# Kernel optimization log

Measured on AMD Instinct MI355X. Metric: run time of the kernel, lower is better.

## Reference

```python
import jax, jax.numpy as jnp
import numpy as np

N = 50000          # num_nodes
E = 1600000        # num directed edges
IN_C = 128         # in_channels
OUT_C = 128        # out_channels
HEADS = 8
HFD = OUT_C // HEADS  # head_feat_dim = 16
NEG_SLOPE = 0.2


def setup_inputs() -> dict:
    key = jax.random.key(0)
    k1, k2, k3, k4, k5 = jax.random.split(key, 5)
    node_feats = jax.random.normal(k1, (N, IN_C), dtype=jnp.float32)
    edge_index = jax.random.randint(k2, (2, E), 0, N, dtype=jnp.int64)
    # parameters (xavier-ish scale, kept small so exp() stays in range)
    W = jax.random.normal(k3, (OUT_C, IN_C), dtype=jnp.float32) * (1.0 / np.sqrt(IN_C))
    a_left = jax.random.normal(k4, (HFD, HEADS), dtype=jnp.float32) * 0.1
    a_right = jax.random.normal(k5, (HFD, HEADS), dtype=jnp.float32) * 0.1
    bias = jnp.zeros((OUT_C,), dtype=jnp.float32)
    return {"node_feats": node_feats, "edge_index": edge_index,
            "W": W, "a_left": a_left, "a_right": a_right, "bias": bias}


def reference(node_feats, edge_index, W, a_left, a_right, bias):
    n = node_feats.shape[0]
    # embedding: Linear without bias, then split into heads -> [n, h, c]
    emb = (node_feats @ W.T).reshape(n, HEADS, HFD)
    # per-node attention logit halves: sum_c emb[n,h,c] * a[c,h] -> [n, h]
    left = jnp.einsum('nhc,ch->nh', emb, a_left)
    right = jnp.einsum('nhc,ch->nh', emb, a_right)
    src = edge_index[0]
    dst = edge_index[1]
    # edge logit: score(src, dst) uses a_left on src, a_right on dst
    e = left[src] + right[dst]                       # [E, h]
    e = jnp.where(e >= 0, e, NEG_SLOPE * e)          # leaky relu(0.2)
    w = jnp.exp(e)                                   # [E, h] (module uses raw exp)
    denom = jax.ops.segment_sum(w, dst, num_segments=n)  # [n, h]
    attn = w / denom[dst]                            # [E, h]
    msg = emb[src] * attn[:, :, None]                # [E, h, c]
    out = jax.ops.segment_sum(msg, dst, num_segments=n)  # [n, h, c]
    # concat heads + bias
    out = out.reshape(n, HEADS * HFD) + bias
    return out
```

## Files before the change

kernel.cpp:

```cpp
#include <hip/hip_runtime.h>
#include <hip/hip_bf16.h>

#define N_NODES 50000
#define N_EDGES 1600000
#define HEADS 8
#define HFD 16
#define CH 128

#define PART 128
#define NB 391
#define BCAP 5120
#define PA_T 512
#define PA_CHUNK 3200
#define PA_PER 7
#define PA_BLOCKS 500
#define EMB_BLOCKS 391

#define QPART 32
#define QCAP 1536
#define AG_TASKS (NB * 4)
#define AG_BLOCKS 1568

typedef __bf16 bf16x8 __attribute__((ext_vector_type(8)));
typedef __bf16 bf16x4 __attribute__((ext_vector_type(4)));
typedef float f32x4 __attribute__((ext_vector_type(4)));
typedef float f32x2 __attribute__((ext_vector_type(2)));

__device__ __forceinline__ float bf_lo(unsigned u) { return __uint_as_float(u << 16); }
__device__ __forceinline__ float bf_hi(unsigned u) { return __uint_as_float(u & 0xffff0000u); }

__global__ __launch_bounds__(256) void k_splitw(const float* __restrict__ W,
                                                const float* __restrict__ aL,
                                                const float* __restrict__ aR,
                                                __bf16* __restrict__ Whi,
                                                __bf16* __restrict__ Wlo,
                                                __bf16* __restrict__ Vhi,
                                                __bf16* __restrict__ Vlo,
                                                int* __restrict__ bucket_cnt) {
  int t = blockIdx.x * 256 + threadIdx.x;
  if (t < NB) bucket_cnt[t] = 0;
  if (t < CH * CH / 4) {
    f32x4 v = ((const f32x4*)W)[t];
    bf16x4 h, l;
#pragma unroll
    for (int i = 0; i < 4; ++i) {
      __bf16 hb = (__bf16)v[i];
      h[i] = hb;
      l[i] = (__bf16)(v[i] - (float)hb);
    }
    ((bf16x4*)Whi)[t] = h;
    ((bf16x4*)Wlo)[t] = l;
  }
  if (t < 16 * CH) {
    int j = t >> 7;
    int k = t & 127;
    int h = j & 7;
    const float* a = (j < 8) ? aL : aR;
    float v = 0.f;
#pragma unroll
    for (int c = 0; c < HFD; ++c) v += W[(h * HFD + c) * CH + k] * a[c * HEADS + h];
    __bf16 hb = (__bf16)v;
    Vhi[t] = hb;
    Vlo[t] = (__bf16)(v - (float)hb);
  }
}

__global__ __launch_bounds__(PA_T) void k_prep(const int* __restrict__ ei,
                                               int* __restrict__ bucket_cnt,
                                               unsigned* __restrict__ ebuf,
                                               const float* __restrict__ X,
                                               const __bf16* __restrict__ Whi,
                                               const __bf16* __restrict__ Wlo,
                                               const __bf16* __restrict__ Vhi,
                                               const __bf16* __restrict__ Vlo,
                                               __bf16* __restrict__ embb,
                                               float* __restrict__ leftp,
                                               float* __restrict__ rightp) {
  __shared__ unsigned sp[PA_CHUNK];
  __shared__ int hist[NB];
  __shared__ int lcur[NB];
  __shared__ int wbase[NB];
  __shared__ int wpart[8];
  int t = threadIdx.x;

  if (blockIdx.x >= PA_BLOCKS) {
    int ntile = (blockIdx.x - PA_BLOCKS) * 8 + (t >> 6);
    if (ntile >= N_NODES / 16) return;
    int lane = t & 63;
    int c = lane & 15, quad = lane >> 4;
    const float* xp = X + (size_t)(ntile * 16 + c) * CH + quad * 8;
    bf16x8 xh[4], xl[4];
#pragma unroll
    for (int ks = 0; ks < 4; ++ks) {
      float4 x0 = *(const float4*)(xp + ks * 32);
      float4 x1 = *(const float4*)(xp + ks * 32 + 4);
      float xv[8] = {x0.x, x0.y, x0.z, x0.w, x1.x, x1.y, x1.z, x1.w};
#pragma unroll
      for (int j = 0; j < 8; ++j) {
        __bf16 hb = (__bf16)xv[j];
        xh[ks][j] = hb;
        xl[ks][j] = (__bf16)(xv[j] - (float)hb);
      }
    }
#pragma unroll
    for (int h = 0; h < HEADS; ++h) {
      const __bf16* wp = Whi + (size_t)(h * 16 + c) * CH + quad * 8;
      const __bf16* wlp = Wlo + (size_t)(h * 16 + c) * CH + quad * 8;
      f32x4 acc = {0.f, 0.f, 0.f, 0.f};
#pragma unroll
      for (int ks = 0; ks < 4; ++ks) {
        bf16x8 wh = *(const bf16x8*)(wp + ks * 32);
        bf16x8 wl = *(const bf16x8*)(wlp + ks * 32);
        acc = __builtin_amdgcn_mfma_f32_16x16x32_bf16(xl[ks], wh, acc, 0, 0, 0);
        acc = __builtin_amdgcn_mfma_f32_16x16x32_bf16(xh[ks], wl, acc, 0, 0, 0);
        acc = __builtin_amdgcn_mfma_f32_16x16x32_bf16(xh[ks], wh, acc, 0, 0, 0);
      }
#pragma unroll
      for (int r = 0; r < 4; ++r) {
        int node = ntile * 16 + quad * 4 + r;
        embb[(size_t)node * CH + h * HFD + c] = (__bf16)acc[r];
      }
    }
    {
      const __bf16* vp = Vhi + (size_t)c * CH + quad * 8;
      const __bf16* vlp = Vlo + (size_t)c * CH + quad * 8;
      f32x4 acc = {0.f, 0.f, 0.f, 0.f};
#pragma unroll
      for (int ks = 0; ks < 4; ++ks) {
        bf16x8 vh = *(const bf16x8*)(vp + ks * 32);
        bf16x8 vl = *(const bf16x8*)(vlp + ks * 32);
        acc = __builtin_amdgcn_mfma_f32_16x16x32_bf16(xl[ks], vh, acc, 0, 0, 0);
        acc = __builtin_amdgcn_mfma_f32_16x16x32_bf16(xh[ks], vl, acc, 0, 0, 0);
        acc = __builtin_amdgcn_mfma_f32_16x16x32_bf16(xh[ks], vh, acc, 0, 0, 0);
      }
#pragma unroll
      for (int r = 0; r < 4; ++r) {
        int node = ntile * 16 + quad * 4 + r;
        if (c < 8) leftp[node * HEADS + c] = acc[r];
        else rightp[node * HEADS + (c - 8)] = acc[r];
      }
    }
    return;
  }

  int base = blockIdx.x * PA_CHUNK;
  for (int i = t; i < NB; i += PA_T) hist[i] = 0;
  __syncthreads();
  unsigned pk[PA_PER];
#pragma unroll
  for (int i = 0; i < PA_PER; ++i) {
    int e = t + i * PA_T;
    pk[i] = 0xffffffffu;
    if (e < PA_CHUNK) {
      int src = ei[base + e];
      int dst = ei[N_EDGES + base + e];
      pk[i] = ((unsigned)(dst >> 7) << 23) | ((unsigned)(dst & 127) << 16) |
              (unsigned)src;
      atomicAdd(&hist[dst >> 7], 1);
    }
  }
  __syncthreads();
  int hv = (t < NB) ? hist[t] : 0;
  int lane = t & 63, wid = t >> 6;
  int v = hv;
#pragma unroll
  for (int d = 1; d < 64; d <<= 1) {
    int o = __shfl_up(v, d);
    if (lane >= d) v += o;
  }
  if (lane == 63) wpart[wid] = v;
  __syncthreads();
  if (t < 8) {
    int pv = wpart[t];
#pragma unroll
    for (int d = 1; d < 8; d <<= 1) {
      int o = __shfl_up(pv, d);
      if (t >= d) pv += o;
    }
    wpart[t] = pv;
  }
  __syncthreads();
  int val = v + ((wid > 0) ? wpart[wid - 1] : 0);
  if (t < NB) {
    int lstart = val - hv;
    lcur[t] = lstart;
    int prior = hv ? atomicAdd(&bucket_cnt[t], hv) : 0;
    wbase[t] = t * BCAP + prior - lstart;
  }
  __syncthreads();
#pragma unroll
  for (int i = 0; i < PA_PER; ++i) {
    if (pk[i] != 0xffffffffu) {
      int b = pk[i] >> 23;
      int pos = atomicAdd(&lcur[b], 1);
      sp[pos] = pk[i];
    }
  }
  __syncthreads();
  for (int i = t; i < PA_CHUNK; i += PA_T) {
    unsigned p = sp[i];
    int b = p >> 23;
    int slot = wbase[b] + i;
    if (slot < (b + 1) * BCAP) ebuf[slot] = p;
  }
}

__global__ __launch_bounds__(256) void k_aggr(const int* __restrict__ bucket_cnt,
                                              const unsigned* __restrict__ ebuf,
                                              const __bf16* __restrict__ embb,
                                              const float* __restrict__ leftp,
                                              const float* __restrict__ rightp,
                                              const float* __restrict__ bias,
                                              float* __restrict__ out) {
  __shared__ unsigned short su[QCAP];
  __shared__ int hist[QPART];
  __shared__ int pfx[QPART];
  __shared__ int cur[QPART];
  int T = (blockIdx.x & 7) * (AG_BLOCKS / 8) + (blockIdx.x >> 3);
  if (T >= AG_TASKS) return;
  int b = T >> 2;
  int q = T & 3;
  int t = threadIdx.x;
  int cnt = bucket_cnt[b];
  if (cnt > BCAP) cnt = BCAP;
  int ebase = b * BCAP;
  if (t < QPART) hist[t] = 0;
  __syncthreads();
  for (int e4 = t * 4; e4 < cnt; e4 += 1024) {
    uint4 pp = *(const uint4*)(ebuf + ebase + e4);
    unsigned pj[4] = {pp.x, pp.y, pp.z, pp.w};
#pragma unroll
    for (int j = 0; j < 4; ++j) {
      if (e4 + j < cnt) {
        int dl = (pj[j] >> 16) & 127;
        if ((dl >> 5) == q) atomicAdd(&hist[dl & 31], 1);
      }
    }
  }
  __syncthreads();
  if (t < 64) {
    int v = (t < QPART) ? hist[t] : 0;
#pragma unroll
    for (int d = 1; d < QPART; d <<= 1) {
      int o = __shfl_up(v, d);
      if (t >= d) v += o;
    }
    if (t < QPART) {
      int ex = v - hist[t];
      pfx[t] = ex;
      cur[t] = ex;
    }
  }
  __syncthreads();
  for (int e4 = t * 4; e4 < cnt; e4 += 1024) {
    uint4 pp = *(const uint4*)(ebuf + ebase + e4);
    unsigned pj[4] = {pp.x, pp.y, pp.z, pp.w};
#pragma unroll
    for (int j = 0; j < 4; ++j) {
      if (e4 + j < cnt) {
        unsigned p = pj[j];
        int dl = (p >> 16) & 127;
        if ((dl >> 5) == q) {
          int pos = atomicAdd(&cur[dl & 31], 1);
          if (pos < QCAP) su[pos] = (unsigned short)(p & 0xffffu);
        }
      }
    }
  }
  __syncthreads();

  int wv = t >> 6;
  int lane = t & 63;
  int g = lane >> 4;
  int m = lane & 15;
  int h = m >> 1;
#pragma unroll 1
  for (int k = 0; k < 8; ++k) {
    int dl = wv * 8 + k;
    int dst = b * PART + q * QPART + dl;
    bool valid = dst < N_NODES;
    int beg = pfx[dl];
    int cd = hist[dl];
    if (beg + cd > QCAP) cd = QCAP - beg;
    float r = valid ? rightp[dst * HEADS + h] : 0.f;
    f32x2 acc2[4];
    acc2[0] = (f32x2){0.f, 0.f};
    acc2[1] = (f32x2){0.f, 0.f};
    acc2[2] = (f32x2){0.f, 0.f};
    acc2[3] = (f32x2){0.f, 0.f};
    float dsum = 0.f;
    if (cd > 0) {
      int sA0, sA1, sB0, sB1, sC0, sC1;
      uint4 uA0, uA1, uB0, uB1, uC0, uC1;
      float lA0, lA1, lB0, lB1, lC0, lC1;
#define STAGE(E0, s0, s1, u0, u1, l0, l1)                          \
      {                                                            \
        int i0 = (E0) + g, i1 = (E0) + 4 + g;                      \
        s0 = su[beg + ((i0 < cd) ? i0 : 0)];                       \
        s1 = su[beg + ((i1 < cd) ? i1 : 0)];                       \
        u0 = ((const uint4*)(embb + (size_t)s0 * CH))[m];          \
        u1 = ((const uint4*)(embb + (size_t)s1 * CH))[m];          \
        l0 = leftp[s0 * HEADS + h];                                \
        l1 = leftp[s1 * HEADS + h];                                \
      }
#define CONSUME(E0, u0, u1, l0, l1)                                \
      {                                                            \
        bool a0 = (E0) + g < cd, a1 = (E0) + 4 + g < cd;           \
        float x0 = l0 + r;                                         \
        x0 = (x0 >= 0.f) ? x0 : 0.2f * x0;                         \
        float w0 = a0 ? __expf(x0) : 0.f;                          \
        float x1 = l1 + r;                                         \
        x1 = (x1 >= 0.f) ? x1 : 0.2f * x1;                         \
        float w1 = a1 ? __expf(x1) : 0.f;                          \
        dsum += w0 + w1;                                           \
        f32x2 wv0 = {w0, w0}, wv1 = {w1, w1};                      \
        acc2[0] += wv0 * (f32x2){bf_lo(u0.x), bf_hi(u0.x)}         \
                 + wv1 * (f32x2){bf_lo(u1.x), bf_hi(u1.x)};        \
        acc2[1] += wv0 * (f32x2){bf_lo(u0.y), bf_hi(u0.y)}         \
                 + wv1 * (f32x2){bf_lo(u1.y), bf_hi(u1.y)};        \
        acc2[2] += wv0 * (f32x2){bf_lo(u0.z), bf_hi(u0.z)}         \
                 + wv1 * (f32x2){bf_lo(u1.z), bf_hi(u1.z)};        \
        acc2[3] += wv0 * (f32x2){bf_lo(u0.w), bf_hi(u0.w)}         \
                 + wv1 * (f32x2){bf_lo(u1.w), bf_hi(u1.w)};        \
      }
      STAGE(0, sA0, sA1, uA0, uA1, lA0, lA1);
      __builtin_amdgcn_sched_barrier(0);
      if (8 < cd) STAGE(8, sB0, sB1, uB0, uB1, lB0, lB1);
      __builtin_amdgcn_sched_barrier(0);
      int e0 = 0;
      while (true) {
        if (e0 + 16 < cd) STAGE(e0 + 16, sC0, sC1, uC0, uC1, lC0, lC1);
        __builtin_amdgcn_sched_barrier(0);
        CONSUME(e0, uA0, uA1, lA0, lA1);
        e0 += 8;
        if (e0 >= cd) break;
        if (e0 + 16 < cd) STAGE(e0 + 16, sA0, sA1, uA0, uA1, lA0, lA1);
        __builtin_amdgcn_sched_barrier(0);
        CONSUME(e0, uB0, uB1, lB0, lB1);
        e0 += 8;
        if (e0 >= cd) break;
        if (e0 + 16 < cd) STAGE(e0 + 16, sB0, sB1, uB0, uB1, lB0, lB1);
        __builtin_amdgcn_sched_barrier(0);
        CONSUME(e0, uC0, uC1, lC0, lC1);
        e0 += 8;
        if (e0 >= cd) break;
      }
#undef STAGE
#undef CONSUME
    }
    float a0 = acc2[0].x, a1 = acc2[0].y, a2 = acc2[1].x, a3 = acc2[1].y;
    float a4 = acc2[2].x, a5 = acc2[2].y, a6 = acc2[3].x, a7 = acc2[3].y;
#pragma unroll
    for (int mask = 16; mask <= 32; mask <<= 1) {
      dsum += __shfl_xor(dsum, mask);
      a0 += __shfl_xor(a0, mask);
      a1 += __shfl_xor(a1, mask);
      a2 += __shfl_xor(a2, mask);
      a3 += __shfl_xor(a3, mask);
      a4 += __shfl_xor(a4, mask);
      a5 += __shfl_xor(a5, mask);
      a6 += __shfl_xor(a6, mask);
      a7 += __shfl_xor(a7, mask);
    }
    if (g == 0 && valid) {
      float inv = (dsum > 0.f) ? 1.0f / dsum : 0.f;
      float4 b0 = ((const float4*)bias)[2 * m];
      float4 b1 = ((const float4*)bias)[2 * m + 1];
      float4 o0 = {a0 * inv + b0.x, a1 * inv + b0.y,
                   a2 * inv + b0.z, a3 * inv + b0.w};
      float4 o1 = {a4 * inv + b1.x, a5 * inv + b1.y,
                   a6 * inv + b1.z, a7 * inv + b1.w};
      ((float4*)(out + (size_t)dst * CH))[2 * m] = o0;
      ((float4*)(out + (size_t)dst * CH))[2 * m + 1] = o1;
    }
  }
}

extern "C" void kernel_launch(void* const* d_in, const int* in_sizes, int n_in,
                              void* d_out, int out_size, void* d_ws, size_t ws_size,
                              hipStream_t stream) {
  const float* X = (const float*)d_in[0];
  const int* ei = (const int*)d_in[1];
  const float* W = (const float*)d_in[2];
  const float* al = (const float*)d_in[3];
  const float* ar = (const float*)d_in[4];
  const float* bias = (const float*)d_in[5];
  float* out = (float*)d_out;

  unsigned* ebuf = (unsigned*)d_ws;
  __bf16* embb = (__bf16*)(ebuf + (size_t)NB * BCAP);
  __bf16* Whi = embb + (size_t)N_NODES * CH;
  __bf16* Wlo = Whi + CH * CH;
  __bf16* Vhi = Wlo + CH * CH;
  __bf16* Vlo = Vhi + 16 * CH;
  float* leftp = (float*)(Vlo + 16 * CH);
  float* rightp = leftp + (size_t)N_NODES * HEADS;
  int* bucket_cnt = (int*)(rightp + (size_t)N_NODES * HEADS);

  k_splitw<<<16, 256, 0, stream>>>(W, al, ar, Whi, Wlo, Vhi, Vlo, bucket_cnt);
  k_prep<<<PA_BLOCKS + EMB_BLOCKS, PA_T, 0, stream>>>(ei, bucket_cnt, ebuf, X,
                                                      Whi, Wlo, Vhi, Vlo, embb,
                                                      leftp, rightp);
  k_aggr<<<AG_BLOCKS, 256, 0, stream>>>(bucket_cnt, ebuf, embb, leftp, rightp, bias, out);
}
```

Measured before the change: 206.4 us.

## Bin aggregation edges by source-node phase to improve gather locality across waves

The aggregation kernel now sorts each quarter-bucket's edges by destination and also by a coarse source-index phase (src>>14, four phases). Every wave keeps accumulators for all 8 of its destinations in registers and walks the phases in order. The aim is for concurrently running waves to gather embedding rows from the same region of memory, which should improve L2/cache hit rates. In exchange, the manual triple-buffered software prefetch pipeline is dropped in favour of a simple per-edge loop. The kernel also now holds 8x4 accumulators per lane and adds launch bounds of 4 blocks, which raises register pressure and the risk of spilling.

```diff
diff --git a/kernel.cpp b/kernel.cpp
--- a/kernel.cpp
+++ b/kernel.cpp
@@ -20,6 +20,10 @@
 #define QCAP 1536
 #define AG_TASKS (NB * 4)
 #define AG_BLOCKS 1568
+
+#define NPH 4
+#define PHSH 14
+#define NBIN (NPH * QPART)
 
 typedef __bf16 bf16x8 __attribute__((ext_vector_type(8)));
 typedef __bf16 bf16x4 __attribute__((ext_vector_type(4)));
@@ -205,17 +209,18 @@
   }
 }
 
-__global__ __launch_bounds__(256) void k_aggr(const int* __restrict__ bucket_cnt,
-                                              const unsigned* __restrict__ ebuf,
-                                              const __bf16* __restrict__ embb,
-                                              const float* __restrict__ leftp,
-                                              const float* __restrict__ rightp,
-                                              const float* __restrict__ bias,
-                                              float* __restrict__ out) {
+__global__ __launch_bounds__(256, 4) void k_aggr(const int* __restrict__ bucket_cnt,
+                                                 const unsigned* __restrict__ ebuf,
+                                                 const __bf16* __restrict__ embb,
+                                                 const float* __restrict__ leftp,
+                                                 const float* __restrict__ rightp,
+                                                 const float* __restrict__ bias,
+                                                 float* __restrict__ out) {
   __shared__ unsigned short su[QCAP];
-  __shared__ int hist[QPART];
-  __shared__ int pfx[QPART];
-  __shared__ int cur[QPART];
+  __shared__ int hist[NBIN];
+  __shared__ int pfx[NBIN];
+  __shared__ int cur[NBIN];
+  __shared__ int wp2[2];
   int T = (blockIdx.x & 7) * (AG_BLOCKS / 8) + (blockIdx.x >> 3);
   if (T >= AG_TASKS) return;
   int b = T >> 2;
@@ -224,7 +229,7 @@
   int cnt = bucket_cnt[b];
   if (cnt > BCAP) cnt = BCAP;
   int ebase = b * BCAP;
-  if (t < QPART) hist[t] = 0;
+  for (int i = t; i < NBIN; i += 256) hist[i] = 0;
   __syncthreads();
   for (int e4 = t * 4; e4 < cnt; e4 += 1024) {
     uint4 pp = *(const uint4*)(ebuf + ebase + e4);
@@ -233,23 +238,31 @@
     for (int j = 0; j < 4; ++j) {
       if (e4 + j < cnt) {
         int dl = (pj[j] >> 16) & 127;
-        if ((dl >> 5) == q) atomicAdd(&hist[dl & 31], 1);
-      }
-    }
-  }
-  __syncthreads();
-  if (t < 64) {
-    int v = (t < QPART) ? hist[t] : 0;
-#pragma unroll
-    for (int d = 1; d < QPART; d <<= 1) {
+        if ((dl >> 5) == q) {
+          int ph = (int)(pj[j] & 0xffffu) >> PHSH;
+          atomicAdd(&hist[ph * QPART + (dl & 31)], 1);
+        }
+      }
+    }
+  }
+  __syncthreads();
+  int hv = 0, vin = 0;
+  if (t < NBIN) {
+    hv = hist[t];
+    int v = hv;
+#pragma unroll
+    for (int d = 1; d < 64; d <<= 1) {
       int o = __shfl_up(v, d);
-      if (t >= d) v += o;
-    }
-    if (t < QPART) {
-      int ex = v - hist[t];
-      pfx[t] = ex;
-      cur[t] = ex;
-    }
+      if ((t & 63) >= d) v += o;
+    }
+    if ((t & 63) == 63) wp2[t >> 6] = v;
+    vin = v;
+  }
+  __syncthreads();
+  if (t < NBIN) {
+    int inc = vin + ((t >= 64) ? wp2[0] : 0);
+    pfx[t] = inc - hv;
+    cur[t] = inc - hv;
   }
   __syncthreads();
   for (int e4 = t * 4; e4 < cnt; e4 += 1024) {
@@ -261,7 +274,8 @@
         unsigned p = pj[j];
         int dl = (p >> 16) & 127;
         if ((dl >> 5) == q) {
-          int pos = atomicAdd(&cur[dl & 31], 1);
+          int ph = (int)(p & 0xffffu) >> PHSH;
+          int pos = atomicAdd(&cur[ph * QPART + (dl & 31)], 1);
           if (pos < QCAP) su[pos] = (unsigned short)(p & 0xffffu);
         }
       }
@@ -274,85 +288,57 @@
   int g = lane >> 4;
   int m = lane & 15;
   int h = m >> 1;
+  int dbase = b * PART + q * QPART + wv * 8;
+
+  f32x2 acc[8][4];
+  float dsum[8];
+  float rr[8];
+#pragma unroll
+  for (int k = 0; k < 8; ++k) {
+    int dst = dbase + k;
+    rr[k] = (dst < N_NODES) ? rightp[dst * HEADS + h] : 0.f;
+    dsum[k] = 0.f;
+#pragma unroll
+    for (int j = 0; j < 4; ++j) acc[k][j] = (f32x2){0.f, 0.f};
+  }
+
 #pragma unroll 1
+  for (int p = 0; p < NPH; ++p) {
+#pragma unroll
+    for (int k = 0; k < 8; ++k) {
+      int bin = p * QPART + wv * 8 + k;
+      int beg = pfx[bin];
+      int cd = hist[bin];
+      if (beg + cd > QCAP) cd = QCAP - beg;
+      for (int e0 = 0; e0 < cd; e0 += 4) {
+        int i0 = e0 + g;
+        bool a0 = i0 < cd;
+        int s0 = su[beg + (a0 ? i0 : 0)];
+        uint4 u0 = ((const uint4*)(embb + (size_t)s0 * CH))[m];
+        float l0 = leftp[s0 * HEADS + h];
+        float x0 = l0 + rr[k];
+        x0 = (x0 >= 0.f) ? x0 : 0.2f * x0;
+        float w0 = a0 ? __expf(x0) : 0.f;
+        dsum[k] += w0;
+        f32x2 wv0 = {w0, w0};
+        acc[k][0] += wv0 * (f32x2){bf_lo(u0.x), bf_hi(u0.x)};
+        acc[k][1] += wv0 * (f32x2){bf_lo(u0.y), bf_hi(u0.y)};
+        acc[k][2] += wv0 * (f32x2){bf_lo(u0.z), bf_hi(u0.z)};
+        acc[k][3] += wv0 * (f32x2){bf_lo(u0.w), bf_hi(u0.w)};
+      }
+    }
+  }
+
+#pragma unroll
   for (int k = 0; k < 8; ++k) {
-    int dl = wv * 8 + k;
-    int dst = b * PART + q * QPART + dl;
-    bool valid = dst < N_NODES;
-    int beg = pfx[dl];
-    int cd = hist[dl];
-    if (beg + cd > QCAP) cd = QCAP - beg;
-    float r = valid ? rightp[dst * HEADS + h] : 0.f;
-    f32x2 acc2[4];
-    acc2[0] = (f32x2){0.f, 0.f};
-    acc2[1] = (f32x2){0.f, 0.f};
-    acc2[2] = (f32x2){0.f, 0.f};
-    acc2[3] = (f32x2){0.f, 0.f};
-    float dsum = 0.f;
-    if (cd > 0) {
-      int sA0, sA1, sB0, sB1, sC0, sC1;
-      uint4 uA0, uA1, uB0, uB1, uC0, uC1;
-      float lA0, lA1, lB0, lB1, lC0, lC1;
-#define STAGE(E0, s0, s1, u0, u1, l0, l1)                          \
-      {                                                            \
-        int i0 = (E0) + g, i1 = (E0) + 4 + g;                      \
-        s0 = su[beg + ((i0 < cd) ? i0 : 0)];                       \
-        s1 = su[beg + ((i1 < cd) ? i1 : 0)];                       \
-        u0 = ((const uint4*)(embb + (size_t)s0 * CH))[m];          \
-        u1 = ((const uint4*)(embb + (size_t)s1 * CH))[m];          \
-        l0 = leftp[s0 * HEADS + h];                                \
-        l1 = leftp[s1 * HEADS + h];                                \
-      }
-#define CONSUME(E0, u0, u1, l0, l1)                                \
-      {                                                            \
-        bool a0 = (E0) + g < cd, a1 = (E0) + 4 + g < cd;           \
-        float x0 = l0 + r;                                         \
-        x0 = (x0 >= 0.f) ? x0 : 0.2f * x0;                         \
-        float w0 = a0 ? __expf(x0) : 0.f;                          \
-        float x1 = l1 + r;                                         \
-        x1 = (x1 >= 0.f) ? x1 : 0.2f * x1;                         \
-        float w1 = a1 ? __expf(x1) : 0.f;                          \
-        dsum += w0 + w1;                                           \
-        f32x2 wv0 = {w0, w0}, wv1 = {w1, w1};                      \
-        acc2[0] += wv0 * (f32x2){bf_lo(u0.x), bf_hi(u0.x)}         \
-                 + wv1 * (f32x2){bf_lo(u1.x), bf_hi(u1.x)};        \
-        acc2[1] += wv0 * (f32x2){bf_lo(u0.y), bf_hi(u0.y)}         \
-                 + wv1 * (f32x2){bf_lo(u1.y), bf_hi(u1.y)};        \
-        acc2[2] += wv0 * (f32x2){bf_lo(u0.z), bf_hi(u0.z)}         \
-                 + wv1 * (f32x2){bf_lo(u1.z), bf_hi(u1.z)};        \
-        acc2[3] += wv0 * (f32x2){bf_lo(u0.w), bf_hi(u0.w)}         \
-                 + wv1 * (f32x2){bf_lo(u1.w), bf_hi(u1.w)};        \
-      }
-      STAGE(0, sA0, sA1, uA0, uA1, lA0, lA1);
-      __builtin_amdgcn_sched_barrier(0);
-      if (8 < cd) STAGE(8, sB0, sB1, uB0, uB1, lB0, lB1);
-      __builtin_amdgcn_sched_barrier(0);
-      int e0 = 0;
-      while (true) {
-        if (e0 + 16 < cd) STAGE(e0 + 16, sC0, sC1, uC0, uC1, lC0, lC1);
-        __builtin_amdgcn_sched_barrier(0);
-        CONSUME(e0, uA0, uA1, lA0, lA1);
-        e0 += 8;
-        if (e0 >= cd) break;
-        if (e0 + 16 < cd) STAGE(e0 + 16, sA0, sA1, uA0, uA1, lA0, lA1);
-        __builtin_amdgcn_sched_barrier(0);
-        CONSUME(e0, uB0, uB1, lB0, lB1);
-        e0 += 8;
-        if (e0 >= cd) break;
-        if (e0 + 16 < cd) STAGE(e0 + 16, sB0, sB1, uB0, uB1, lB0, lB1);
-        __builtin_amdgcn_sched_barrier(0);
-        CONSUME(e0, uC0, uC1, lC0, lC1);
-        e0 += 8;
-        if (e0 >= cd) break;
-      }
-#undef STAGE
-#undef CONSUME
-    }
-    float a0 = acc2[0].x, a1 = acc2[0].y, a2 = acc2[1].x, a3 = acc2[1].y;
-    float a4 = acc2[2].x, a5 = acc2[2].y, a6 = acc2[3].x, a7 = acc2[3].y;
+    int dst = dbase + k;
+    float ds = dsum[k];
+    ds += __shfl_xor(ds, 16);
+    ds += __shfl_xor(ds, 32);
+    float a0 = acc[k][0].x, a1 = acc[k][0].y, a2 = acc[k][1].x, a3 = acc[k][1].y;
+    float a4 = acc[k][2].x, a5 = acc[k][2].y, a6 = acc[k][3].x, a7 = acc[k][3].y;
 #pragma unroll
     for (int mask = 16; mask <= 32; mask <<= 1) {
-      dsum += __shfl_xor(dsum, mask);
       a0 += __shfl_xor(a0, mask);
       a1 += __shfl_xor(a1, mask);
       a2 += __shfl_xor(a2, mask);
@@ -362,8 +348,8 @@
       a6 += __shfl_xor(a6, mask);
       a7 += __shfl_xor(a7, mask);
     }
-    if (g == 0 && valid) {
-      float inv = (dsum > 0.f) ? 1.0f / dsum : 0.f;
+    if (g == 0 && dst < N_NODES) {
+      float inv = (ds > 0.f) ? 1.0f / ds : 0.f;
       float4 b0 = ((const float4*)bias)[2 * m];
       float4 b1 = ((const float4*)bias)[2 * m + 1];
       float4 o0 = {a0 * inv + b0.x, a1 * inv + b0.y,
```

Result: slower. 231.6 us (+12.2%).
